# Optimization experiments

Hardware: AMD Instinct MI355X
Metric: run time of the kernel (lower is better)

Reference implementation:

```python
import jax, jax.numpy as jnp
import numpy as np

N = 4096      # nodes
E = 131072    # edges (avg degree 32)
H = 4         # attention heads
D_IN = 128
D_H = 256     # per-head out features
ALPHA = 0.2   # LeakyReLU slope


def setup_inputs() -> dict:
    key = jax.random.key(0)
    ks = jax.random.split(key, 12)
    p = lambda k, shape: jax.random.normal(k, shape, dtype=jnp.float32) * 0.05
    return {
        "x": jax.random.normal(ks[0], (N, D_IN), dtype=jnp.float32),
        "edge_index": jax.random.randint(ks[1], (2, E), 0, N),
        "Wp": p(ks[2], (D_IN, D_H)),
        "bp": jnp.zeros((D_H,), jnp.float32),
        "W0": p(ks[3], (H, D_H, D_H)),
        "a0": p(ks[4], (H, 2 * D_H)),
        "W1": p(ks[5], (H, H * D_H, D_H)),
        "a1": p(ks[6], (H, 2 * D_H)),
        "W2": p(ks[7], (H, H * D_H, D_H)),
        "a2": p(ks[8], (H, 2 * D_H)),
        "pool_w": p(ks[9], (H * D_H, 1)),
        "pool_b": jnp.zeros((1,), jnp.float32),
        "c1_w": p(ks[10], (H * D_H, D_H)),
        "c1_b": jnp.zeros((D_H,), jnp.float32),
        "c2_w": p(ks[11], (D_H, 7)),
        "c2_b": jnp.zeros((7,), jnp.float32),
    }


def _gat_layer(h, W, a, src, dst):
    # h: [N, in]; W: [H, in, out]; a: [H, 2*out]
    n = h.shape[0]
    out = W.shape[-1]
    Wh = jnp.einsum('ni,hio->hno', h, W)                      # [H, N, out]
    e_src = jnp.einsum('ho,hno->hn', a[:, :out], Wh)          # a . Wh_src part
    e_dst = jnp.einsum('ho,hno->hn', a[:, out:], Wh)          # a . Wh_dst part
    e = jax.nn.leaky_relu(e_src[:, src] + e_dst[:, dst], ALPHA)  # [H, E]
    # Faithful to original: dense NxN scatter, softmax over rows INCLUDING
    # the implicit zeros at non-edge positions (exp(0)=1 contributes).
    attn = jnp.zeros((W.shape[0], n, n), h.dtype).at[:, src, dst].set(e)
    attn = jax.nn.softmax(attn, axis=2)                       # [H, N, N]
    importance = attn.sum(axis=1).sum(axis=0)                 # sum over heads of col-sums
    h_prime = jax.nn.elu(jnp.einsum('hnm,hmo->hno', attn, Wh))
    # concat heads -> [N, H*out]
    return h_prime.transpose(1, 0, 2).reshape(n, -1), importance


def reference(x, edge_index, Wp, bp, W0, a0, W1, a1, W2, a2,
              pool_w, pool_b, c1_w, c1_b, c2_w, c2_b):
    src, dst = edge_index[0], edge_index[1]
    h = jax.nn.relu(x @ Wp + bp)                              # [N, D_H]
    total_importance = jnp.zeros((x.shape[0],), x.dtype)
    for W, a in ((W0, a0), (W1, a1), (W2, a2)):
        h, imp = _gat_layer(h, W, a, src, dst)
        total_importance = total_importance + imp
    node_attention = total_importance / (3 * H)
    attn_w = jax.nn.softmax(h @ pool_w + pool_b, axis=0)      # [N, 1]
    graph_emb = (attn_w * h).sum(axis=0, keepdims=True)       # [1, H*D_H]
    logits = jax.nn.relu(graph_emb @ c1_w + c1_b) @ c2_w + c2_b
    probs = jax.nn.softmax(logits, axis=-1)                   # [1, 7]
    return probs, node_attention
```

## Files before the change

### kernel.cpp

```cpp
#include <hip/hip_runtime.h>
#include <hip/hip_bf16.h>
#include <math.h>

#define NN   4096
#define EE   131072
#define HH   4
#define DIN  128
#define DH   256
#define DCAT 1024
#define ALPHA_LR 0.2f

typedef __attribute__((ext_vector_type(8))) short  short8;
typedef __attribute__((ext_vector_type(4))) short  s16x4;
typedef __attribute__((ext_vector_type(4))) float  f32x4;

__device__ __forceinline__ unsigned short f2bf(float f) {
    union { float f; unsigned u; } v; v.f = f;
    unsigned r = v.u + 0x7fffu + ((v.u >> 16) & 1u);
    return (unsigned short)(r >> 16);
}
__device__ __forceinline__ float bf2f(unsigned short us) {
    union { unsigned u; float f; } v; v.u = ((unsigned)us) << 16;
    return v.f;
}

__global__ void prep_kernel(const float* __restrict__ x, unsigned short* __restrict__ xb,
                            const float* __restrict__ Wp, unsigned short* __restrict__ BTp,
                            const float* __restrict__ W0, unsigned short* __restrict__ BT0,
                            const float* __restrict__ W1, unsigned short* __restrict__ BT1,
                            const float* __restrict__ W2, unsigned short* __restrict__ BT2,
                            const int* __restrict__ src, const int* __restrict__ dst,
                            int* __restrict__ counts, int* __restrict__ counts2)
{
    __shared__ float tile[32][33];
    const int b = blockIdx.x, tid = threadIdx.x;
    if (b < 512) {
        int i = b * 256 + tid;
        f32x4 v = *(const f32x4*)(x + (size_t)i * 4);
        s16x4 o;
        o[0] = (short)f2bf(v[0]); o[1] = (short)f2bf(v[1]);
        o[2] = (short)f2bf(v[2]); o[3] = (short)f2bf(v[3]);
        *(s16x4*)(xb + (size_t)i * 4) = o;
        return;
    }
    if (b >= 2848) {
        int e = (b - 2848) * 256 + tid;
        atomicAdd(&counts[src[e]], 1);
        atomicAdd(&counts2[dst[e]], 1);
        return;
    }
    const float* W; unsigned short* BT; int K, h, kt, ot;
    if (b < 544)       { int c = b - 512;  W = Wp; BT = BTp; K = DIN;  h = 0;      kt = c & 3;  ot = c >> 2; }
    else if (b < 800)  { int c = b - 544;  W = W0; BT = BT0; K = DH;   h = c >> 6; kt = c & 7;  ot = (c >> 3) & 7; }
    else if (b < 1824) { int c = b - 800;  W = W1; BT = BT1; K = DCAT; h = c >> 8; kt = c & 31; ot = (c >> 5) & 7; }
    else               { int c = b - 1824; W = W2; BT = BT2; K = DCAT; h = c >> 8; kt = c & 31; ot = (c >> 5) & 7; }
    int k0 = kt * 32, o0 = ot * 32;
    int tx = tid & 31, ty = tid >> 5;
    const float* Ws = W + (size_t)h * K * 256;
#pragma unroll
    for (int i = 0; i < 32; i += 8)
        tile[ty + i][tx] = Ws[(size_t)(k0 + ty + i) * 256 + o0 + tx];
    __syncthreads();
#pragma unroll
    for (int i = 0; i < 32; i += 8)
        BT[(size_t)(h * 256 + o0 + ty + i) * K + k0 + tx] = f2bf(tile[tx][ty + i]);
}

__global__ __launch_bounds__(256)
void mfma_gemm_kernel(const unsigned short* __restrict__ A,
                      const unsigned short* __restrict__ BT,
                      int K,
                      unsigned short* __restrict__ Cb,
                      int ldc, int head_major,
                      const float* __restrict__ bias, int relu_act,
                      const float* __restrict__ av,
                      float* __restrict__ es4, float* __restrict__ ed4,
                      float* __restrict__ csum)
{
    __shared__ __align__(16) unsigned short sA[2][128 * 32];
    __shared__ __align__(16) unsigned short sB[2][128 * 32];

    const int tid = threadIdx.x;
    const int w = tid >> 6, l = tid & 63;
    const int wr = w >> 1, wc = w & 1;
    const int row0 = blockIdx.x * 128, col0 = blockIdx.y * 128;
    const int lrow = l >> 2;
    const int lce  = (l & 3) * 8;
    const int lr = l & 15, lg = l >> 4;

    f32x4 acc[4][4];
#pragma unroll
    for (int m = 0; m < 4; ++m)
#pragma unroll
        for (int n = 0; n < 4; ++n)
            acc[m][n] = (f32x4){0.f, 0.f, 0.f, 0.f};

#define STAGE(buf, k0)                                                          \
    {                                                                           \
        _Pragma("unroll")                                                       \
        for (int p = 0; p < 2; ++p) {                                           \
            int chunk = w * 2 + p;                                              \
            int r = chunk * 16 + lrow;                                          \
            const unsigned short* ga = A  + (size_t)(row0 + r) * K + (k0) + lce;\
            const unsigned short* gb = BT + (size_t)(col0 + r) * K + (k0) + lce;\
            __builtin_amdgcn_global_load_lds(                                   \
                (const __attribute__((address_space(1))) unsigned int*)ga,      \
                (__attribute__((address_space(3))) unsigned int*)(&sA[buf][chunk * 512]), \
                16, 0, 0);                                                      \
            __builtin_amdgcn_global_load_lds(                                   \
                (const __attribute__((address_space(1))) unsigned int*)gb,      \
                (__attribute__((address_space(3))) unsigned int*)(&sB[buf][chunk * 512]), \
                16, 0, 0);                                                      \
        }                                                                       \
    }

#define COMPUTE(buf)                                                            \
    {                                                                           \
        short8 af[4], bfr[4];                                                   \
        _Pragma("unroll")                                                       \
        for (int m = 0; m < 4; ++m) {                                           \
            int r = wr * 64 + m * 16 + lr;                                      \
            af[m] = *(const short8*)(&sA[buf][r * 32 + lg * 8]);                \
        }                                                                       \
        _Pragma("unroll")                                                       \
        for (int n = 0; n < 4; ++n) {                                           \
            int r = wc * 64 + n * 16 + lr;                                      \
            bfr[n] = *(const short8*)(&sB[buf][r * 32 + lg * 8]);               \
        }                                                                       \
        _Pragma("unroll")                                                       \
        for (int m = 0; m < 4; ++m)                                             \
            _Pragma("unroll")                                                   \
            for (int n = 0; n < 4; ++n)                                         \
                acc[m][n] = __builtin_amdgcn_mfma_f32_16x16x32_bf16(            \
                    af[m], bfr[n], acc[m][n], 0, 0, 0);                         \
    }

    STAGE(0, 0);
    __syncthreads();
    int nt = K >> 5, cur = 0;
    for (int t = 0; t < nt - 1; ++t) {
        STAGE(cur ^ 1, (t + 1) * 32);
        COMPUTE(cur);
        __syncthreads();
        cur ^= 1;
    }
    COMPUTE(cur);
#undef STAGE
#undef COMPUTE

#pragma unroll
    for (int m = 0; m < 4; ++m) {
        int rbase = row0 + wr * 64 + m * 16 + lg * 4;
#pragma unroll
        for (int n = 0; n < 4; ++n) {
            int c = col0 + wc * 64 + n * 16 + lr;
            float bv = bias ? bias[c] : 0.f;
#pragma unroll
            for (int r = 0; r < 4; ++r) {
                float v = acc[m][n][r] + bv;
                if (relu_act) v = fmaxf(v, 0.f);
                size_t idx = head_major
                    ? (size_t)(c >> 8) * ((size_t)NN * DH) + (size_t)(rbase + r) * DH + (c & 255)
                    : (size_t)(rbase + r) * ldc + c;
                Cb[idx] = f2bf(v);
            }
        }
    }

    if (av) {
        const int h = (col0 + wc * 64) >> 8;
        float aes[4], aed[4];
#pragma unroll
        for (int n = 0; n < 4; ++n) {
            int cc = (col0 + wc * 64 + n * 16 + lr) & 255;
            aes[n] = av[h * 2 * DH + cc];
            aed[n] = av[h * 2 * DH + DH + cc];
        }
#pragma unroll
        for (int m = 0; m < 4; ++m) {
#pragma unroll
            for (int r = 0; r < 4; ++r) {
                float se = 0.f, sd = 0.f;
#pragma unroll
                for (int n = 0; n < 4; ++n) {
                    se = fmaf(aes[n], acc[m][n][r], se);
                    sd = fmaf(aed[n], acc[m][n][r], sd);
                }
                se += __shfl_xor(se, 1);  sd += __shfl_xor(sd, 1);
                se += __shfl_xor(se, 2);  sd += __shfl_xor(sd, 2);
                se += __shfl_xor(se, 4);  sd += __shfl_xor(sd, 4);
                se += __shfl_xor(se, 8);  sd += __shfl_xor(sd, 8);
                if (lr == 0) {
                    int row = row0 + wr * 64 + m * 16 + lg * 4 + r;
                    atomicAdd(&es4[row * 4 + h], se);
                    atomicAdd(&ed4[row * 4 + h], sd);
                }
            }
        }
#pragma unroll
        for (int n = 0; n < 4; ++n) {
            float s = 0.f;
#pragma unroll
            for (int m = 0; m < 4; ++m)
#pragma unroll
                for (int r = 0; r < 4; ++r)
                    s += acc[m][n][r];
            s += __shfl_xor(s, 16);
            s += __shfl_xor(s, 32);
            if (lg == 0) atomicAdd(&csum[col0 + wc * 64 + n * 16 + lr], s);
        }
    }
}

__global__ void scan2_kernel(const int* __restrict__ countsA, const int* __restrict__ countsB,
                             int* __restrict__ rowptr, int* __restrict__ cursor,
                             int* __restrict__ cscptr, int* __restrict__ ccursor)
{
    __shared__ int lsumA[1024];
    __shared__ int lsumB[1024];
    int t = threadIdx.x;
    int base = t * 4;
    int a0 = countsA[base], a1 = countsA[base + 1], a2 = countsA[base + 2], a3 = countsA[base + 3];
    int b0 = countsB[base], b1 = countsB[base + 1], b2 = countsB[base + 2], b3 = countsB[base + 3];
    int sA = a0 + a1 + a2 + a3;
    int sB = b0 + b1 + b2 + b3;
    lsumA[t] = sA; lsumB[t] = sB;
    __syncthreads();
    for (int off = 1; off < 1024; off <<= 1) {
        int vA = (t >= off) ? lsumA[t - off] : 0;
        int vB = (t >= off) ? lsumB[t - off] : 0;
        __syncthreads();
        lsumA[t] += vA; lsumB[t] += vB;
        __syncthreads();
    }
    int eA = lsumA[t] - sA;
    rowptr[base] = eA;               cursor[base] = eA;
    rowptr[base + 1] = eA + a0;      cursor[base + 1] = eA + a0;
    rowptr[base + 2] = eA + a0 + a1; cursor[base + 2] = eA + a0 + a1;
    rowptr[base + 3] = eA + a0 + a1 + a2; cursor[base + 3] = eA + a0 + a1 + a2;
    int eB = lsumB[t] - sB;
    cscptr[base] = eB;               ccursor[base] = eB;
    cscptr[base + 1] = eB + b0;      ccursor[base + 1] = eB + b0;
    cscptr[base + 2] = eB + b0 + b1; ccursor[base + 2] = eB + b0 + b1;
    cscptr[base + 3] = eB + b0 + b1 + b2; ccursor[base + 3] = eB + b0 + b1 + b2;
    if (t == 1023) { rowptr[NN] = lsumA[1023]; cscptr[NN] = lsumB[1023]; }
}

__global__ void fill_kernel(const int* __restrict__ src, const int* __restrict__ dst,
                            int* __restrict__ cursor, int* __restrict__ ccursor,
                            int* __restrict__ cdst, int* __restrict__ cscpos)
{
    int e = blockIdx.x * 256 + threadIdx.x;
    int s = src[e], d = dst[e];
    int pos = atomicAdd(&cursor[s], 1);
    cdst[pos] = d;
    int cp = atomicAdd(&ccursor[d], 1);
    cscpos[cp] = pos;
}

__global__ __launch_bounds__(256)
void edgew_kernel(const float* __restrict__ es, const float* __restrict__ ed,
                  const int* __restrict__ rowptr, const int* __restrict__ cdst,
                  float* __restrict__ wpk,
                  float* __restrict__ invd4,
                  float* __restrict__ wi)
{
    const int wave = threadIdx.x >> 6, lane = threadIdx.x & 63;
    const int n = blockIdx.x * 4 + wave;
    const int beg = rowptr[n], end = rowptr[n + 1];
    const int deg = end - beg;
    const float es0 = es[n * 4 + 0], es1 = es[n * 4 + 1];
    const float es2 = es[n * 4 + 2], es3 = es[n * 4 + 3];

    float sw0 = 0.f, sw1 = 0.f, sw2 = 0.f, sw3 = 0.f;
    for (int i = lane; i < deg; i += 64) {
        int d = cdst[beg + i];
        f32x4 ev = *(const f32x4*)(ed + d * 4);
        float v0 = es0 + ev[0]; v0 = v0 > 0.f ? v0 : ALPHA_LR * v0;
        float v1 = es1 + ev[1]; v1 = v1 > 0.f ? v1 : ALPHA_LR * v1;
        float v2 = es2 + ev[2]; v2 = v2 > 0.f ? v2 : ALPHA_LR * v2;
        float v3 = es3 + ev[3]; v3 = v3 > 0.f ? v3 : ALPHA_LR * v3;
        float w0 = expm1f(v0), w1 = expm1f(v1), w2 = expm1f(v2), w3 = expm1f(v3);
        sw0 += w0; sw1 += w1; sw2 += w2; sw3 += w3;
        wpk[beg + i] = w0;
        wpk[EE + beg + i] = w1;
        wpk[2 * EE + beg + i] = w2;
        wpk[3 * EE + beg + i] = w3;
    }
#pragma unroll
    for (int off = 32; off; off >>= 1) {
        sw0 += __shfl_xor(sw0, off);
        sw1 += __shfl_xor(sw1, off);
        sw2 += __shfl_xor(sw2, off);
        sw3 += __shfl_xor(sw3, off);
    }
    const float iv0 = 1.f / ((float)NN + sw0);
    const float iv1 = 1.f / ((float)NN + sw1);
    const float iv2 = 1.f / ((float)NN + sw2);
    const float iv3 = 1.f / ((float)NN + sw3);
    if (lane == 0)
        *(f32x4*)(invd4 + n * 4) = (f32x4){iv0, iv1, iv2, iv3};
    for (int i = lane; i < deg; i += 64) {
        float w0 = wpk[beg + i], w1 = wpk[EE + beg + i];
        float w2 = wpk[2 * EE + beg + i], w3 = wpk[3 * EE + beg + i];
        wi[beg + i] = fmaf(w0, iv0, fmaf(w1, iv1, fmaf(w2, iv2, w3 * iv3)));
    }
}

__global__ void ctot_reduce_kernel(const float* __restrict__ invd4_3, float* __restrict__ Ctot)
{
    float s = 0.f;
    for (int i = blockIdx.x * 256 + threadIdx.x; i < 3 * NN * 4; i += gridDim.x * 256)
        s += invd4_3[i];
#pragma unroll
    for (int off = 32; off; off >>= 1) s += __shfl_down(s, off);
    if ((threadIdx.x & 63) == 0) atomicAdd(Ctot, s);
}

__global__ __launch_bounds__(256)
void gather_kernel(const unsigned short* __restrict__ Whb,
                   const float* __restrict__ wpk, const int* __restrict__ rowptr,
                   const int* __restrict__ cdst, const float* __restrict__ invd4,
                   const float* __restrict__ csum,
                   unsigned short* __restrict__ hb_out,
                   const float* __restrict__ pwp, float* __restrict__ ps4)
{
    __shared__ float red[4][DH];
    const int b = blockIdx.x;
    const int xcd = b & 7;
    const int h = xcd >> 1;
    const int n = (b >> 3) + (xcd & 1) * (NN / 2);
    const int tid = threadIdx.x;
    const int w = tid >> 6, lane = tid & 63;
    const int slot = lane >> 5;
    const int c8 = (lane & 31) * 8;
    const int beg = rowptr[n], end = rowptr[n + 1];
    const int deg = end - beg;
    const float* wph = wpk + (size_t)h * EE;
    const unsigned short* basep = Whb + (size_t)h * NN * DH + c8;

    float acc[8] = {};
    for (int i0 = w * 8; i0 < deg; i0 += 32) {
        float ww[4]; int dd[4];
#pragma unroll
        for (int p = 0; p < 4; ++p) {
            int e = i0 + p * 2 + slot;
            int ec = e < deg ? e : (deg - 1);
            ww[p] = (e < deg) ? wph[beg + ec] : 0.f;
            dd[p] = cdst[beg + ec];
        }
        short8 vv[4];
#pragma unroll
        for (int p = 0; p < 4; ++p)
            vv[p] = *(const short8*)(basep + (size_t)dd[p] * DH);
#pragma unroll
        for (int p = 0; p < 4; ++p)
#pragma unroll
            for (int j = 0; j < 8; ++j)
                acc[j] = fmaf(ww[p], bf2f((unsigned short)vv[p][j]), acc[j]);
    }
#pragma unroll
    for (int j = 0; j < 8; ++j) acc[j] += __shfl_xor(acc[j], 32);
    if (lane < 32) {
        *(f32x4*)(&red[w][c8])     = (f32x4){acc[0], acc[1], acc[2], acc[3]};
        *(f32x4*)(&red[w][c8 + 4]) = (f32x4){acc[4], acc[5], acc[6], acc[7]};
    }
    __syncthreads();

    if (tid < 64) {
        const float iv = invd4[n * 4 + h];
        f32x4 s0 = *(const f32x4*)(&red[0][tid * 4]);
        f32x4 s1 = *(const f32x4*)(&red[1][tid * 4]);
        f32x4 s2 = *(const f32x4*)(&red[2][tid * 4]);
        f32x4 s3 = *(const f32x4*)(&red[3][tid * 4]);
        f32x4 cs = *(const f32x4*)(&csum[h * DH + tid * 4]);
        f32x4 r;
        s16x4 ob;
#pragma unroll
        for (int j = 0; j < 4; ++j) {
            float v = (cs[j] + s0[j] + s1[j] + s2[j] + s3[j]) * iv;
            v = v > 0.f ? v : expm1f(v);
            r[j] = v;
            ob[j] = (short)f2bf(v);
        }
        *(s16x4*)(&hb_out[(size_t)n * DCAT + h * DH + tid * 4]) = ob;
        if (pwp) {
            f32x4 pv = *(const f32x4*)(&pwp[h * DH + tid * 4]);
            float p = r[0] * pv[0] + r[1] * pv[1] + r[2] * pv[2] + r[3] * pv[3];
#pragma unroll
            for (int off = 32; off; off >>= 1) p += __shfl_down(p, off);
            if (tid == 0) ps4[n * 4 + h] = p;
        }
    }
}

__global__ void impgather_kernel(const int* __restrict__ cscptr, const int* __restrict__ cscpos,
                                 const float* __restrict__ wi0, const float* __restrict__ wi1,
                                 const float* __restrict__ wi2, const float* __restrict__ Ctot,
                                 float* __restrict__ out)
{
    int gid = blockIdx.x * 256 + threadIdx.x;
    int m = gid >> 3;
    int l = gid & 7;
    int beg = cscptr[m], end = cscptr[m + 1];
    float s = 0.f;
    for (int j = beg + l; j < end; j += 8) {
        int p = cscpos[j];
        s += wi0[p] + wi1[p] + wi2[p];
    }
    s += __shfl_down(s, 4, 8);
    s += __shfl_down(s, 2, 8);
    s += __shfl_down(s, 1, 8);
    if (l == 0) out[7 + m] = (s + Ctot[0]) * (1.0f / 12.0f);
}

__global__ void emb_kernel(const unsigned short* __restrict__ h3, const float* __restrict__ ps4,
                           float* __restrict__ emb)
{
    __shared__ float red[8];
    __shared__ float MM, SS;
    __shared__ float pawl[256];
    int t = threadIdx.x;
    float m = -1e30f;
    for (int i = t; i < NN; i += 256) {
        f32x4 q = *(const f32x4*)(ps4 + i * 4);
        m = fmaxf(m, q[0] + q[1] + q[2] + q[3]);
    }
#pragma unroll
    for (int off = 32; off; off >>= 1) m = fmaxf(m, __shfl_down(m, off));
    if ((t & 63) == 0) red[t >> 6] = m;
    __syncthreads();
    if (t == 0) MM = fmaxf(fmaxf(red[0], red[1]), fmaxf(red[2], red[3]));
    __syncthreads();
    float s = 0.f;
    for (int i = t; i < NN; i += 256) {
        f32x4 q = *(const f32x4*)(ps4 + i * 4);
        s += expf(q[0] + q[1] + q[2] + q[3] - MM);
    }
#pragma unroll
    for (int off = 32; off; off >>= 1) s += __shfl_down(s, off);
    __syncthreads();
    if ((t & 63) == 0) red[t >> 6] = s;
    __syncthreads();
    if (t == 0) SS = red[0] + red[1] + red[2] + red[3];
    __syncthreads();
    int n0 = blockIdx.y * 256;
    {
        f32x4 q = *(const f32x4*)(ps4 + (n0 + t) * 4);
        pawl[t] = expf(q[0] + q[1] + q[2] + q[3] - MM) / SS;
    }
    __syncthreads();
    float a0 = 0.f, a1 = 0.f, a2 = 0.f, a3 = 0.f;
    for (int j = 0; j < 256; ++j) {
        float pw = pawl[j];
        s16x4 v = *(const s16x4*)(&h3[(size_t)(n0 + j) * DCAT + t * 4]);
        a0 = fmaf(pw, bf2f((unsigned short)v[0]), a0);
        a1 = fmaf(pw, bf2f((unsigned short)v[1]), a1);
        a2 = fmaf(pw, bf2f((unsigned short)v[2]), a2);
        a3 = fmaf(pw, bf2f((unsigned short)v[3]), a3);
    }
    atomicAdd(&emb[t * 4 + 0], a0);
    atomicAdd(&emb[t * 4 + 1], a1);
    atomicAdd(&emb[t * 4 + 2], a2);
    atomicAdd(&emb[t * 4 + 3], a3);
}

__global__ void c1_kernel(const float* __restrict__ emb, const float* __restrict__ c1w,
                          float* __restrict__ zbuf)
{
    int t = threadIdx.x;
    int r0 = blockIdx.x * 32;
    float s = 0.f;
#pragma unroll
    for (int j = 0; j < 32; ++j)
        s = fmaf(emb[r0 + j], c1w[(size_t)(r0 + j) * DH + t], s);
    atomicAdd(&zbuf[t], s);
}

__global__ void c2_kernel(const float* __restrict__ zbuf, const float* __restrict__ c1b,
                          const float* __restrict__ c2w, const float* __restrict__ c2b,
                          float* __restrict__ out)
{
    __shared__ float z[DH];
    __shared__ float lgs[8];
    int t = threadIdx.x;
    z[t] = fmaxf(zbuf[t] + c1b[t], 0.f);
    __syncthreads();
    int g = t >> 5, k = t & 31;
    if (g < 7) {
        float s = 0.f;
#pragma unroll
        for (int j = 0; j < 8; ++j)
            s = fmaf(z[k + 32 * j], c2w[(k + 32 * j) * 7 + g], s);
#pragma unroll
        for (int off = 16; off; off >>= 1) s += __shfl_down(s, off, 32);
        if (k == 0) lgs[g] = s + c2b[g];
    }
    __syncthreads();
    if (t == 0) {
        float m = lgs[0];
        for (int i = 1; i < 7; ++i) m = fmaxf(m, lgs[i]);
        float sm = 0.f, ex[7];
        for (int i = 0; i < 7; ++i) { ex[i] = expf(lgs[i] - m); sm += ex[i]; }
        for (int i = 0; i < 7; ++i) out[i] = ex[i] / sm;
    }
}

extern "C" void kernel_launch(void* const* d_in, const int* in_sizes, int n_in,
                              void* d_out, int out_size, void* d_ws, size_t ws_size,
                              hipStream_t stream)
{
    const float* x   = (const float*)d_in[0];
    const int*   ei  = (const int*)d_in[1];
    const float* Wp  = (const float*)d_in[2];
    const float* bp  = (const float*)d_in[3];
    const float* W[3]  = {(const float*)d_in[4], (const float*)d_in[6], (const float*)d_in[8]};
    const float* av[3] = {(const float*)d_in[5], (const float*)d_in[7], (const float*)d_in[9]};
    const float* pw  = (const float*)d_in[10];
    const float* c1w = (const float*)d_in[12];
    const float* c1b = (const float*)d_in[13];
    const float* c2w = (const float*)d_in[14];
    const float* c2b = (const float*)d_in[15];
    float* out = (float*)d_out;
    (void)in_sizes; (void)n_in; (void)out_size; (void)ws_size;

    char* base = (char*)d_ws;
    size_t off = 0;
    auto alloc = [&](size_t bytes) -> void* {
        void* p = base + off;
        off = (off + bytes + 255) & ~(size_t)255;
        return p;
    };
    size_t zero_begin = off;
    float* es4_3 = (float*)alloc((size_t)3 * NN * 16);
    float* ed4_3 = (float*)alloc((size_t)3 * NN * 16);
    float* csum3 = (float*)alloc((size_t)3 * DCAT * 4);
    float* Ctot  = (float*)alloc(256);
    int*   counts  = (int*)alloc(NN * 4);
    int*   counts2 = (int*)alloc(NN * 4);
    float* emb   = (float*)alloc(DCAT * 4);
    float* zbuf  = (float*)alloc(DH * 4);
    size_t zero_bytes = off - zero_begin;
    unsigned short* xb   = (unsigned short*)alloc((size_t)NN * DIN * 2);
    unsigned short* BTp  = (unsigned short*)alloc((size_t)DH * DIN * 2);
    unsigned short* BT0  = (unsigned short*)alloc((size_t)DCAT * DH * 2);
    unsigned short* BT1  = (unsigned short*)alloc((size_t)DCAT * DCAT * 2);
    unsigned short* BT2  = (unsigned short*)alloc((size_t)DCAT * DCAT * 2);
    unsigned short* Whb  = (unsigned short*)alloc((size_t)NN * DCAT * 2);
    unsigned short* hb0  = (unsigned short*)alloc((size_t)NN * DCAT * 2);
    unsigned short* hb1  = (unsigned short*)alloc((size_t)NN * DCAT * 2);
    int*   rowptr  = (int*)alloc((NN + 1) * 4);
    int*   cursor  = (int*)alloc(NN * 4);
    int*   cscptr  = (int*)alloc((NN + 1) * 4);
    int*   ccursor = (int*)alloc(NN * 4);
    int*   cdst    = (int*)alloc((size_t)EE * 4);
    int*   cscpos  = (int*)alloc((size_t)EE * 4);
    float* wi3     = (float*)alloc((size_t)3 * EE * 4);
    float* wpk     = (float*)alloc((size_t)HH * EE * 4);
    float* invd4_3 = (float*)alloc((size_t)3 * NN * 16);
    float* ps4     = (float*)alloc((size_t)NN * 16);

    const int* srcp = ei;
    const int* dstp = ei + EE;

    hipMemsetAsync(base + zero_begin, 0, zero_bytes, stream);

    prep_kernel<<<3360, 256, 0, stream>>>(x, xb, Wp, BTp, W[0], BT0, W[1], BT1, W[2], BT2,
                                          srcp, dstp, counts, counts2);
    scan2_kernel<<<1, 1024, 0, stream>>>(counts, counts2, rowptr, cursor, cscptr, ccursor);
    fill_kernel<<<EE / 256, 256, 0, stream>>>(srcp, dstp, cursor, ccursor, cdst, cscpos);

    mfma_gemm_kernel<<<dim3(NN / 128, DH / 128), 256, 0, stream>>>(
        xb, BTp, DIN, hb0, DH, 0, bp, 1, nullptr, nullptr, nullptr, nullptr);

    unsigned short* cur = hb0;
    unsigned short* nxt = hb1;
    const unsigned short* BTl[3] = {BT0, BT1, BT2};
    for (int layer = 0; layer < 3; ++layer) {
        int K = (layer == 0) ? DH : DCAT;
        float* es = es4_3 + (size_t)layer * NN * 4;
        float* ed = ed4_3 + (size_t)layer * NN * 4;
        float* csum = csum3 + (size_t)layer * DCAT;
        float* wi = wi3 + (size_t)layer * EE;
        float* invd4 = invd4_3 + (size_t)layer * NN * 4;
        mfma_gemm_kernel<<<dim3(NN / 128, DCAT / 128), 256, 0, stream>>>(
            cur, BTl[layer], K, Whb, DCAT, 1, nullptr, 0, av[layer], es, ed, csum);
        edgew_kernel<<<NN / 4, 256, 0, stream>>>(es, ed, rowptr, cdst, wpk, invd4, wi);
        gather_kernel<<<NN * HH, 256, 0, stream>>>(Whb, wpk, rowptr, cdst, invd4, csum, nxt,
                                                   (layer == 2) ? pw : nullptr, ps4);
        unsigned short* t = cur; cur = nxt; nxt = t;
    }

    ctot_reduce_kernel<<<24, 256, 0, stream>>>(invd4_3, Ctot);

    emb_kernel<<<dim3(1, 16), 256, 0, stream>>>(cur, ps4, emb);
    c1_kernel<<<32, 256, 0, stream>>>(emb, c1w, zbuf);
    c2_kernel<<<1, 256, 0, stream>>>(zbuf, c1b, c2w, c2b, out);

    impgather_kernel<<<NN * 8 / 256, 256, 0, stream>>>(cscptr, cscpos,
        wi3, wi3 + EE, wi3 + 2 * EE, Ctot, out);
}
```

Baseline: 280.0 us.

## Fuse edge-weight softmax computation into per-head gather kernel via LDS

Removes the separate edgew_kernel: each gather block now computes its head's leaky-relu/expm1 edge weights for its node, reduces the row sum in-block, normalizes, and keeps the weights in LDS (with a recompute fallback beyond 256 edges). Normalized per-head weights are written per layer, and the importance gather sums 12 arrays with 16 lanes per node instead of a precombined per-layer sum. This saves three kernel launches and the global round trip of the weights, but adds two block barriers and a serial weight phase before the gather, plus more reads in the importance pass.

Measured after the change: 302.2 us. 1.08x slower.

```diff
diff --git a/kernel.cpp b/kernel.cpp
--- a/kernel.cpp
+++ b/kernel.cpp
@@ -9,6 +9,7 @@
 #define DH   256
 #define DCAT 1024
 #define ALPHA_LR 0.2f
+#define MAXDEG 256
 
 typedef __attribute__((ext_vector_type(8))) short  short8;
 typedef __attribute__((ext_vector_type(4))) short  s16x4;
@@ -258,55 +259,6 @@
     cscpos[cp] = pos;
 }
 
-__global__ __launch_bounds__(256)
-void edgew_kernel(const float* __restrict__ es, const float* __restrict__ ed,
-                  const int* __restrict__ rowptr, const int* __restrict__ cdst,
-                  float* __restrict__ wpk,
-                  float* __restrict__ invd4,
-                  float* __restrict__ wi)
-{
-    const int wave = threadIdx.x >> 6, lane = threadIdx.x & 63;
-    const int n = blockIdx.x * 4 + wave;
-    const int beg = rowptr[n], end = rowptr[n + 1];
-    const int deg = end - beg;
-    const float es0 = es[n * 4 + 0], es1 = es[n * 4 + 1];
-    const float es2 = es[n * 4 + 2], es3 = es[n * 4 + 3];
-
-    float sw0 = 0.f, sw1 = 0.f, sw2 = 0.f, sw3 = 0.f;
-    for (int i = lane; i < deg; i += 64) {
-        int d = cdst[beg + i];
-        f32x4 ev = *(const f32x4*)(ed + d * 4);
-        float v0 = es0 + ev[0]; v0 = v0 > 0.f ? v0 : ALPHA_LR * v0;
-        float v1 = es1 + ev[1]; v1 = v1 > 0.f ? v1 : ALPHA_LR * v1;
-        float v2 = es2 + ev[2]; v2 = v2 > 0.f ? v2 : ALPHA_LR * v2;
-        float v3 = es3 + ev[3]; v3 = v3 > 0.f ? v3 : ALPHA_LR * v3;
-        float w0 = expm1f(v0), w1 = expm1f(v1), w2 = expm1f(v2), w3 = expm1f(v3);
-        sw0 += w0; sw1 += w1; sw2 += w2; sw3 += w3;
-        wpk[beg + i] = w0;
-        wpk[EE + beg + i] = w1;
-        wpk[2 * EE + beg + i] = w2;
-        wpk[3 * EE + beg + i] = w3;
-    }
-#pragma unroll
-    for (int off = 32; off; off >>= 1) {
-        sw0 += __shfl_xor(sw0, off);
-        sw1 += __shfl_xor(sw1, off);
-        sw2 += __shfl_xor(sw2, off);
-        sw3 += __shfl_xor(sw3, off);
-    }
-    const float iv0 = 1.f / ((float)NN + sw0);
-    const float iv1 = 1.f / ((float)NN + sw1);
-    const float iv2 = 1.f / ((float)NN + sw2);
-    const float iv3 = 1.f / ((float)NN + sw3);
-    if (lane == 0)
-        *(f32x4*)(invd4 + n * 4) = (f32x4){iv0, iv1, iv2, iv3};
-    for (int i = lane; i < deg; i += 64) {
-        float w0 = wpk[beg + i], w1 = wpk[EE + beg + i];
-        float w2 = wpk[2 * EE + beg + i], w3 = wpk[3 * EE + beg + i];
-        wi[beg + i] = fmaf(w0, iv0, fmaf(w1, iv1, fmaf(w2, iv2, w3 * iv3)));
-    }
-}
-
 __global__ void ctot_reduce_kernel(const float* __restrict__ invd4_3, float* __restrict__ Ctot)
 {
     float s = 0.f;
@@ -319,26 +271,60 @@
 
 __global__ __launch_bounds__(256)
 void gather_kernel(const unsigned short* __restrict__ Whb,
-                   const float* __restrict__ wpk, const int* __restrict__ rowptr,
-                   const int* __restrict__ cdst, const float* __restrict__ invd4,
+                   const float* __restrict__ es, const float* __restrict__ ed,
+                   const int* __restrict__ rowptr, const int* __restrict__ cdst,
                    const float* __restrict__ csum,
+                   float* __restrict__ wpkl,
+                   float* __restrict__ invd4,
                    unsigned short* __restrict__ hb_out,
                    const float* __restrict__ pwp, float* __restrict__ ps4)
 {
+    __shared__ float wlds[MAXDEG];
     __shared__ float red[4][DH];
+    __shared__ float swred[4];
     const int b = blockIdx.x;
     const int xcd = b & 7;
     const int h = xcd >> 1;
     const int n = (b >> 3) + (xcd & 1) * (NN / 2);
     const int tid = threadIdx.x;
     const int w = tid >> 6, lane = tid & 63;
+    const int beg = rowptr[n], end = rowptr[n + 1];
+    const int deg = end - beg;
+    const float esh = es[n * 4 + h];
+
+    float sw = 0.f;
+    for (int i = tid; i < deg; i += 256) {
+        int d = cdst[beg + i];
+        float v = esh + ed[d * 4 + h];
+        v = v > 0.f ? v : ALPHA_LR * v;
+        float wv = expm1f(v);
+        sw += wv;
+        if (i < MAXDEG) wlds[i] = wv;
+    }
+#pragma unroll
+    for (int off = 32; off; off >>= 1) sw += __shfl_xor(sw, off);
+    if (lane == 0) swred[w] = sw;
+    __syncthreads();
+    const float iv = 1.f / ((float)NN + swred[0] + swred[1] + swred[2] + swred[3]);
+    if (tid == 0) invd4[n * 4 + h] = iv;
+    for (int i = tid; i < deg; i += 256) {
+        float wv;
+        if (i < MAXDEG) wv = wlds[i];
+        else {
+            int d = cdst[beg + i];
+            float v = esh + ed[d * 4 + h];
+            v = v > 0.f ? v : ALPHA_LR * v;
+            wv = expm1f(v);
+        }
+        float wiv = wv * iv;
+        wpkl[beg + i] = wiv;
+        if (i < MAXDEG) wlds[i] = wiv;
+    }
+    __syncthreads();
+
     const int slot = lane >> 5;
     const int c8 = (lane & 31) * 8;
-    const int beg = rowptr[n], end = rowptr[n + 1];
-    const int deg = end - beg;
-    const float* wph = wpk + (size_t)h * EE;
     const unsigned short* basep = Whb + (size_t)h * NN * DH + c8;
-
     float acc[8] = {};
     for (int i0 = w * 8; i0 < deg; i0 += 32) {
         float ww[4]; int dd[4];
@@ -346,8 +332,15 @@
         for (int p = 0; p < 4; ++p) {
             int e = i0 + p * 2 + slot;
             int ec = e < deg ? e : (deg - 1);
-            ww[p] = (e < deg) ? wph[beg + ec] : 0.f;
             dd[p] = cdst[beg + ec];
+            if (e < deg) {
+                if (e < MAXDEG) ww[p] = wlds[e];
+                else {
+                    float v = esh + ed[dd[p] * 4 + h];
+                    v = v > 0.f ? v : ALPHA_LR * v;
+                    ww[p] = expm1f(v) * iv;
+                }
+            } else ww[p] = 0.f;
         }
         short8 vv[4];
 #pragma unroll
@@ -368,7 +361,6 @@
     __syncthreads();
 
     if (tid < 64) {
-        const float iv = invd4[n * 4 + h];
         f32x4 s0 = *(const f32x4*)(&red[0][tid * 4]);
         f32x4 s1 = *(const f32x4*)(&red[1][tid * 4]);
         f32x4 s2 = *(const f32x4*)(&red[2][tid * 4]);
@@ -378,7 +370,7 @@
         s16x4 ob;
 #pragma unroll
         for (int j = 0; j < 4; ++j) {
-            float v = (cs[j] + s0[j] + s1[j] + s2[j] + s3[j]) * iv;
+            float v = cs[j] * iv + s0[j] + s1[j] + s2[j] + s3[j];
             v = v > 0.f ? v : expm1f(v);
             r[j] = v;
             ob[j] = (short)f2bf(v);
@@ -395,22 +387,25 @@
 }
 
 __global__ void impgather_kernel(const int* __restrict__ cscptr, const int* __restrict__ cscpos,
-                                 const float* __restrict__ wi0, const float* __restrict__ wi1,
-                                 const float* __restrict__ wi2, const float* __restrict__ Ctot,
+                                 const float* __restrict__ wpk3, const float* __restrict__ Ctot,
                                  float* __restrict__ out)
 {
     int gid = blockIdx.x * 256 + threadIdx.x;
-    int m = gid >> 3;
-    int l = gid & 7;
+    int m = gid >> 4;
+    int l = gid & 15;
     int beg = cscptr[m], end = cscptr[m + 1];
     float s = 0.f;
-    for (int j = beg + l; j < end; j += 8) {
+    for (int j = beg + l; j < end; j += 16) {
         int p = cscpos[j];
-        s += wi0[p] + wi1[p] + wi2[p];
-    }
-    s += __shfl_down(s, 4, 8);
-    s += __shfl_down(s, 2, 8);
-    s += __shfl_down(s, 1, 8);
+        float t = 0.f;
+#pragma unroll
+        for (int q = 0; q < 12; ++q) t += wpk3[(size_t)q * EE + p];
+        s += t;
+    }
+    s += __shfl_down(s, 8, 16);
+    s += __shfl_down(s, 4, 16);
+    s += __shfl_down(s, 2, 16);
+    s += __shfl_down(s, 1, 16);
     if (l == 0) out[7 + m] = (s + Ctot[0]) * (1.0f / 12.0f);
 }
 
@@ -555,8 +550,7 @@
     int*   ccursor = (int*)alloc(NN * 4);
     int*   cdst    = (int*)alloc((size_t)EE * 4);
     int*   cscpos  = (int*)alloc((size_t)EE * 4);
-    float* wi3     = (float*)alloc((size_t)3 * EE * 4);
-    float* wpk     = (float*)alloc((size_t)HH * EE * 4);
+    float* wpk3    = (float*)alloc((size_t)3 * HH * EE * 4);
     float* invd4_3 = (float*)alloc((size_t)3 * NN * 16);
     float* ps4     = (float*)alloc((size_t)NN * 16);
 
@@ -581,12 +575,12 @@
         float* es = es4_3 + (size_t)layer * NN * 4;
         float* ed = ed4_3 + (size_t)layer * NN * 4;
         float* csum = csum3 + (size_t)layer * DCAT;
-        float* wi = wi3 + (size_t)layer * EE;
+        float* wpkl = wpk3 + (size_t)layer * HH * EE;
         float* invd4 = invd4_3 + (size_t)layer * NN * 4;
         mfma_gemm_kernel<<<dim3(NN / 128, DCAT / 128), 256, 0, stream>>>(
             cur, BTl[layer], K, Whb, DCAT, 1, nullptr, 0, av[layer], es, ed, csum);
-        edgew_kernel<<<NN / 4, 256, 0, stream>>>(es, ed, rowptr, cdst, wpk, invd4, wi);
-        gather_kernel<<<NN * HH, 256, 0, stream>>>(Whb, wpk, rowptr, cdst, invd4, csum, nxt,
+        gather_kernel<<<NN * HH, 256, 0, stream>>>(Whb, es, ed, rowptr, cdst, csum,
+                                                   wpkl, invd4, nxt,
                                                    (layer == 2) ? pw : nullptr, ps4);
         unsigned short* t = cur; cur = nxt; nxt = t;
     }
@@ -597,6 +591,5 @@
     c1_kernel<<<32, 256, 0, stream>>>(emb, c1w, zbuf);
     c2_kernel<<<1, 256, 0, stream>>>(zbuf, c1b, c2w, c2b, out);
 
-    impgather_kernel<<<NN * 8 / 256, 256, 0, stream>>>(cscptr, cscpos,
-        wi3, wi3 + EE, wi3 + 2 * EE, Ctot, out);
-}
+    impgather_kernel<<<NN * 16 / 256, 256, 0, stream>>>(cscptr, cscpos, wpk3, Ctot, out);
+}
```
